# Performance work log

Hardware: AMD Instinct MI355X
Metric: run time of the kernel (lower is better)

## Reference

```python
import jax, jax.numpy as jnp
import numpy as np

N_NODES = 50000
N_EDGES = 800000
IN_DIM = 256
OUT_DIM = 64


def setup_inputs() -> dict:
    key = jax.random.key(0)
    k1, k2, k3, k4, k5 = jax.random.split(key, 5)
    h = jax.random.normal(k1, (N_NODES, IN_DIM), dtype=jnp.float32)
    # fc: Linear(in_dim, out_dim, bias=False) -> weight shape [out_dim, in_dim]
    W_fc = jax.random.normal(k2, (OUT_DIM, IN_DIM), dtype=jnp.float32) / np.sqrt(IN_DIM)
    # attn_fc: Linear(2*out_dim, 1, bias=False) -> weight shape [1, 2*out_dim]
    W_attn = jax.random.normal(k3, (1, 2 * OUT_DIM), dtype=jnp.float32) / np.sqrt(2 * OUT_DIM)
    src = jax.random.randint(k4, (N_EDGES,), 0, N_NODES, dtype=jnp.int64 if jax.config.read('jax_enable_x64') else jnp.int32).astype(jnp.int32)
    dst = jax.random.randint(k5, (N_EDGES,), 0, N_NODES, dtype=jnp.int32)
    return {"h": h, "W_fc": W_fc, "W_attn": W_attn, "src": src, "dst": dst}


def reference(h, W_fc, W_attn, src, dst):
    # z = self.fc(h)
    z = h @ W_fc.T                              # [N, D]
    # edge_attention: e = leaky_relu(attn_fc(cat(z_src, z_dst)))
    z_src = z[src]                              # [E, D] gather
    z_dst = z[dst]                              # [E, D] gather
    z2 = jnp.concatenate([z_src, z_dst], axis=1)  # [E, 2D]
    e = jax.nn.leaky_relu(z2 @ W_attn.T)[:, 0]  # [E], torch default slope 0.01
    # reduce_func: segment softmax over incoming edges per dst node
    n = h.shape[0]
    m = jax.ops.segment_max(e, dst, num_segments=n)        # [N] per-node max
    e_exp = jnp.exp(e - m[dst])                             # [E] stable exp
    denom = jax.ops.segment_sum(e_exp, dst, num_segments=n)  # [N]
    alpha = e_exp / jnp.maximum(denom, 1e-16)[dst]          # [E]
    # h' = sum_j alpha_ij * z_j
    out = jax.ops.segment_sum(alpha[:, None] * z_src, dst, num_segments=n)  # [N, D]
    return out
```

## Files before the change

kernel.cpp:

```cpp
#include <hip/hip_runtime.h>

#define N_NODES 50000
#define N_EDGES 800000
#define IN_DIM  256
#define OUT_DIM 64
#define BINW    128
#define NBINS   512
#define NBINS_USED ((N_NODES + BINW - 1) / BINW)
#define PB      112
#define CH4     ((N_EDGES / 4 + PB - 1) / PB)
#define NB_GEMM ((N_NODES + 63) / 64)
#define GRID_FUSED 896
#define CSRCAP  4096

typedef _Float16 f16;
typedef __attribute__((ext_vector_type(2))) __fp16 hf16x2;
typedef __attribute__((ext_vector_type(4))) _Float16 f16x4;
typedef __attribute__((ext_vector_type(8))) _Float16 f16x8;
typedef __attribute__((ext_vector_type(4))) float f32x4;

__device__ __forceinline__ unsigned int pack_sw(int s, float w) {
    f16 hw = (f16)w;
    unsigned short us;
    __builtin_memcpy(&us, &hw, 2);
    return ((unsigned int)s << 16) | us;
}
__device__ __forceinline__ float unpack_w(unsigned int e) {
    unsigned short us = (unsigned short)(e & 0xffffu);
    f16 hw;
    __builtin_memcpy(&hw, &us, 2);
    return (float)hw;
}


__global__ __launch_bounds__(256) void k_prep(const float* __restrict__ W,
                                              f16* __restrict__ Wh,
                                              int* __restrict__ binCount) {
    int idx = blockIdx.x * 256 + threadIdx.x;
    if (idx < (OUT_DIM * IN_DIM) / 4) {
        float4 v = ((const float4*)W)[idx];
        f16x4 p = { (f16)v.x, (f16)v.y, (f16)v.z, (f16)v.w };
        ((f16x4*)Wh)[idx] = p;
    }
    if (idx < NBINS) binCount[idx] = 0;
}

__global__ __launch_bounds__(256) void k_fused(const float* __restrict__ h,
                                               const f16* __restrict__ Wh,
                                               const float* __restrict__ Wa,
                                               const int* __restrict__ dst,
                                               f16* __restrict__ z,
                                               float* __restrict__ a_src,
                                               float* __restrict__ a_dst,
                                               int* __restrict__ binCount,
                                               int* __restrict__ base) {
    __shared__ int hist[NBINS];
    const int g = blockIdx.x;
    const int t = threadIdx.x;

    if ((g & 7) == 7) {
        const int pb = g >> 3;
        for (int b = t; b < NBINS; b += 256) hist[b] = 0;
        __syncthreads();
        const int s4 = pb * CH4;
        const int e4 = min(s4 + CH4, N_EDGES / 4);
        for (int i4 = s4 + t; i4 < e4; i4 += 256) {
            int4 dv = ((const int4*)dst)[i4];
            atomicAdd(&hist[dv.x >> 7], 1);
            atomicAdd(&hist[dv.y >> 7], 1);
            atomicAdd(&hist[dv.z >> 7], 1);
            atomicAdd(&hist[dv.w >> 7], 1);
        }
        __syncthreads();
        for (int b = t; b < NBINS; b += 256) {
            int c = hist[b];
            if (c) base[pb * NBINS + b] = atomicAdd(&binCount[b], c);
        }
        return;
    }

    const int gemm_id = g - (g >> 3);
    if (gemm_id >= NB_GEMM) return;

    const int row0  = gemm_id * 64;
    const int lane  = t & 63;
    const int wid   = t >> 6;
    const int cl    = lane & 15;
    const int khalf = lane >> 4;

    int arow = row0 + wid * 16 + cl;
    if (arow >= N_NODES) arow = N_NODES - 1;
    const float* hrow = h + (size_t)arow * IN_DIM;

    f32x4 acc[4] = {};

    #pragma unroll 4
    for (int kc = 0; kc < IN_DIM; kc += 32) {
        const int k0 = kc + khalf * 8;
        float4 va = *(const float4*)&hrow[k0];
        float4 vb = *(const float4*)&hrow[k0 + 4];
        union { hf16x2 h2[4]; f16x8 h8; } ua;
        ua.h2[0] = __builtin_amdgcn_cvt_pkrtz(va.x, va.y);
        ua.h2[1] = __builtin_amdgcn_cvt_pkrtz(va.z, va.w);
        ua.h2[2] = __builtin_amdgcn_cvt_pkrtz(vb.x, vb.y);
        ua.h2[3] = __builtin_amdgcn_cvt_pkrtz(vb.z, vb.w);
        f16x8 a = ua.h8;
        #pragma unroll
        for (int ct = 0; ct < 4; ++ct) {
            const int col = ct * 16 + cl;
            f16x8 b = *(const f16x8*)&Wh[col * 256 + k0];
            acc[ct] = __builtin_amdgcn_mfma_f32_16x16x32_f16(a, b, acc[ct], 0, 0, 0);
        }
    }

    const int rbase = row0 + wid * 16 + khalf * 4;
    #pragma unroll
    for (int ct = 0; ct < 4; ++ct) {
        #pragma unroll
        for (int r = 0; r < 4; ++r) {
            int row = rbase + r;
            if (row < N_NODES)
                z[(size_t)row * OUT_DIM + ct * 16 + cl] = (f16)acc[ct][r];
        }
    }

    float wa1[4], wa2[4];
    #pragma unroll
    for (int ct = 0; ct < 4; ++ct) {
        wa1[ct] = Wa[ct * 16 + cl];
        wa2[ct] = Wa[64 + ct * 16 + cl];
    }
    #pragma unroll
    for (int r = 0; r < 4; ++r) {
        float s1 = 0.f, s2 = 0.f;
        #pragma unroll
        for (int ct = 0; ct < 4; ++ct) {
            s1 += acc[ct][r] * wa1[ct];
            s2 += acc[ct][r] * wa2[ct];
        }
        #pragma unroll
        for (int off = 1; off < 16; off <<= 1) {
            s1 += __shfl_xor(s1, off);
            s2 += __shfl_xor(s2, off);
        }
        int row = rbase + r;
        if (cl == 0 && row < N_NODES) {
            a_src[row] = s1;
            a_dst[row] = s2;
        }
    }
}

__global__ __launch_bounds__(256) void k_place(const int* __restrict__ src,
                                               const int* __restrict__ dst,
                                               const int* __restrict__ binCount,
                                               const int* __restrict__ base,
                                               int* __restrict__ ebuf) {
    __shared__ int cursor[NBINS];
    const int pb = blockIdx.x;
    const int t  = threadIdx.x;

    if (t < 64) {
        int vals[8]; int run = 0;
        #pragma unroll
        for (int i = 0; i < 8; ++i) { int c = binCount[t * 8 + i]; vals[i] = run; run += c; }
        int incl = run;
        #pragma unroll
        for (int off = 1; off < 64; off <<= 1) {
            int u = __shfl_up(incl, off);
            if (t >= off) incl += u;
        }
        const int lex = incl - run;
        #pragma unroll
        for (int i = 0; i < 8; ++i) cursor[t * 8 + i] = lex + vals[i];
    }
    __syncthreads();
    for (int b = t; b < NBINS; b += 256) cursor[b] += base[pb * NBINS + b];
    __syncthreads();

    const int s4 = pb * CH4;
    const int e4 = min(s4 + CH4, N_EDGES / 4);
    for (int i4 = s4 + t; i4 < e4; i4 += 256) {
        int4 dv = ((const int4*)dst)[i4];
        int4 sv = ((const int4*)src)[i4];
        int slot;
        slot = atomicAdd(&cursor[dv.x >> 7], 1); ebuf[slot] = (sv.x << 7) | (dv.x & 127);
        slot = atomicAdd(&cursor[dv.y >> 7], 1); ebuf[slot] = (sv.y << 7) | (dv.y & 127);
        slot = atomicAdd(&cursor[dv.z >> 7], 1); ebuf[slot] = (sv.z << 7) | (dv.z & 127);
        slot = atomicAdd(&cursor[dv.w >> 7], 1); ebuf[slot] = (sv.w << 7) | (dv.w & 127);
    }
}

__global__ __launch_bounds__(1024) void k_binagg(const int* __restrict__ ebuf,
                                                 const int* __restrict__ binCount,
                                                 const float* __restrict__ a_src,
                                                 const float* __restrict__ a_dst,
                                                 const f16* __restrict__ z,
                                                 float* __restrict__ out) {
    __shared__ int cnt[BINW];
    __shared__ int rb[BINW];
    __shared__ int cur[BINW];
    __shared__ float adl[BINW];
    __shared__ unsigned int lcsr[CSRCAP];
    __shared__ int sh_estart;
    const int b    = blockIdx.x;
    const int t    = threadIdx.x;
    const int lane = t & 63;
    const int wid  = t >> 6;
    const int node0 = b * BINW;
    const int ecnt  = min(binCount[b], CSRCAP);

    if (t < 64) {
        int partial = 0;
        for (int i = t; i < b; i += 64) partial += binCount[i];
        #pragma unroll
        for (int off = 32; off; off >>= 1) partial += __shfl_xor(partial, off);
        if (t == 0) sh_estart = partial;
    }
    if (t < BINW) {
        cnt[t] = 0;
        int gd = node0 + t;
        adl[t] = (gd < N_NODES) ? a_dst[gd] : 0.f;
    }
    __syncthreads();
    const int estart = sh_estart;

    for (int i = t; i < ecnt; i += 1024)
        atomicAdd(&cnt[ebuf[estart + i] & (BINW - 1)], 1);
    __syncthreads();

    if (t < 64) {
        int v0 = cnt[t], v1 = cnt[t + 64];
        int i0 = v0;
        #pragma unroll
        for (int off = 1; off < 64; off <<= 1) {
            int u = __shfl_up(i0, off);
            if (t >= off) i0 += u;
        }
        int tot0 = __shfl(i0, 63);
        int i1 = v1;
        #pragma unroll
        for (int off = 1; off < 64; off <<= 1) {
            int u = __shfl_up(i1, off);
            if (t >= off) i1 += u;
        }
        int e0 = i0 - v0;
        int e1 = tot0 + i1 - v1;
        rb[t]       = e0;  cur[t]      = e0;
        rb[t + 64]  = e1;  cur[t + 64] = e1;
    }
    __syncthreads();

    for (int i = t; i < ecnt; i += 1024) {
        int pk = ebuf[estart + i];
        int ld = pk & (BINW - 1);
        int s  = pk >> 7;
        float u = a_src[s] + adl[ld];
        u = u > 0.f ? u : 0.01f * u;
        float w = __expf(u);
        int p = atomicAdd(&cur[ld], 1);
        lcsr[p] = pack_sw(s, w);
    }
    __syncthreads();

    const int grp = lane >> 3;
    const int cl  = lane & 7;
    #pragma unroll
    for (int i = 0; i < 8; ++i) {
        const int ld   = i * 16 + wid;
        const int node = node0 + ld;
        if (node >= N_NODES) continue;
        const int beg = rb[ld];
        const int deg = cnt[ld];

        float dn = 0.0f;
        float acc8[8] = {0.f, 0.f, 0.f, 0.f, 0.f, 0.f, 0.f, 0.f};

        for (int cb = 0; cb < deg; cb += 64) {
            const int rem = min(deg - cb, 64);
            if (lane < rem) dn += unpack_w(lcsr[beg + cb + lane]);
            const int kmax = (rem + 7) & ~7;
            for (int k = 0; k < kmax; k += 8) {
                const int ei = k + grp;
                unsigned int pe = (ei < rem) ? lcsr[beg + cb + ei] : 0u;
                int   sk = (int)(pe >> 16);
                float wk = unpack_w(pe);
                f16x8 zv = *(const f16x8*)&z[(size_t)sk * OUT_DIM + cl * 8];
                #pragma unroll
                for (int j = 0; j < 8; ++j)
                    acc8[j] = fmaf(wk, (float)zv[j], acc8[j]);
            }
        }

        #pragma unroll
        for (int off = 32; off; off >>= 1) dn += __shfl_xor(dn, off);
        #pragma unroll
        for (int off = 8; off < 64; off <<= 1) {
            #pragma unroll
            for (int j = 0; j < 8; ++j)
                acc8[j] += __shfl_xor(acc8[j], off);
        }

        if (lane < 8) {
            float inv = 1.0f / fmaxf(dn, 1e-16f);
            float4 o0 = make_float4(acc8[0] * inv, acc8[1] * inv, acc8[2] * inv, acc8[3] * inv);
            float4 o1 = make_float4(acc8[4] * inv, acc8[5] * inv, acc8[6] * inv, acc8[7] * inv);
            *(float4*)&out[(size_t)node * OUT_DIM + lane * 8]     = o0;
            *(float4*)&out[(size_t)node * OUT_DIM + lane * 8 + 4] = o1;
        }
    }
}


extern "C" void kernel_launch(void* const* d_in, const int* in_sizes, int n_in,
                              void* d_out, int out_size, void* d_ws, size_t ws_size,
                              hipStream_t stream) {
    const float* h      = (const float*)d_in[0];
    const float* W_fc   = (const float*)d_in[1];
    const float* W_attn = (const float*)d_in[2];
    const int*   src    = (const int*)d_in[3];
    const int*   dst    = (const int*)d_in[4];
    float* out = (float*)d_out;

    f16*   z        = (f16*)d_ws;
    f16*   Wh       = z + (size_t)N_NODES * OUT_DIM;
    float* a_src    = (float*)(Wh + OUT_DIM * IN_DIM);
    float* a_dst    = a_src + N_NODES;
    int*   binCount = (int*)(a_dst + N_NODES);
    int*   base     = binCount + NBINS;
    int*   ebuf     = base + PB * NBINS;

    k_prep<<<16, 256, 0, stream>>>(W_fc, Wh, binCount);
    k_fused<<<GRID_FUSED, 256, 0, stream>>>(h, Wh, W_attn, dst, z, a_src, a_dst, binCount, base);
    k_place<<<PB, 256, 0, stream>>>(src, dst, binCount, base, ebuf);
    k_binagg<<<NBINS_USED, 1024, 0, stream>>>(ebuf, binCount, a_src, a_dst, z, out);
}
```

Baseline: 79.94 us.

## Move histogram into prep kernel and fuse edge placement into GEMM kernel

The per-chunk dst histogram moves into the first kernel, which also converts W to fp16. The edge-placement pass then runs inside the fused GEMM kernel's spare blocks, with each block redundantly summing all chunk histograms to build its cursors. This removes one kernel launch and lets placement overlap the GEMM, and bin start/total arrays are written once for the aggregation kernel. The cost is that each placement block reads all PB×NBINS counts and scans them redundantly.

Measured after the change: 86.49 us. +8.2%, slower.

```diff
diff --git a/kernel.cpp b/kernel.cpp
--- a/kernel.cpp
+++ b/kernel.cpp
@@ -33,48 +33,112 @@
 }
 
 
-__global__ __launch_bounds__(256) void k_prep(const float* __restrict__ W,
-                                              f16* __restrict__ Wh,
-                                              int* __restrict__ binCount) {
-    int idx = blockIdx.x * 256 + threadIdx.x;
-    if (idx < (OUT_DIM * IN_DIM) / 4) {
-        float4 v = ((const float4*)W)[idx];
-        f16x4 p = { (f16)v.x, (f16)v.y, (f16)v.z, (f16)v.w };
-        ((f16x4*)Wh)[idx] = p;
-    }
-    if (idx < NBINS) binCount[idx] = 0;
+__global__ __launch_bounds__(1024) void k_prephist(const float* __restrict__ W,
+                                                   const int* __restrict__ dst,
+                                                   f16* __restrict__ Wh,
+                                                   int* __restrict__ base) {
+    const int g = blockIdx.x;
+    const int t = threadIdx.x;
+
+    if (g >= PB) {
+        int idx = (g - PB) * 1024 + t;
+        if (idx < (OUT_DIM * IN_DIM) / 4) {
+            float4 v = ((const float4*)W)[idx];
+            f16x4 p = { (f16)v.x, (f16)v.y, (f16)v.z, (f16)v.w };
+            ((f16x4*)Wh)[idx] = p;
+        }
+        return;
+    }
+
+    __shared__ int hist[NBINS];
+    if (t < NBINS) hist[t] = 0;
+    __syncthreads();
+    const int s4 = g * CH4;
+    const int e4 = min(s4 + CH4, N_EDGES / 4);
+    for (int i4 = s4 + t; i4 < e4; i4 += 1024) {
+        int4 dv = ((const int4*)dst)[i4];
+        atomicAdd(&hist[dv.x >> 7], 1);
+        atomicAdd(&hist[dv.y >> 7], 1);
+        atomicAdd(&hist[dv.z >> 7], 1);
+        atomicAdd(&hist[dv.w >> 7], 1);
+    }
+    __syncthreads();
+    if (t < NBINS) base[g * NBINS + t] = hist[t];
 }
 
 __global__ __launch_bounds__(256) void k_fused(const float* __restrict__ h,
                                                const f16* __restrict__ Wh,
                                                const float* __restrict__ Wa,
+                                               const int* __restrict__ src,
                                                const int* __restrict__ dst,
                                                f16* __restrict__ z,
                                                float* __restrict__ a_src,
                                                float* __restrict__ a_dst,
-                                               int* __restrict__ binCount,
-                                               int* __restrict__ base) {
-    __shared__ int hist[NBINS];
+                                               const int* __restrict__ base,
+                                               int* __restrict__ binStartG,
+                                               int* __restrict__ binTotalG,
+                                               int* __restrict__ ebuf) {
+    __shared__ int cursor[NBINS];
+    __shared__ int totalL[NBINS];
+    __shared__ int bstart[NBINS];
     const int g = blockIdx.x;
     const int t = threadIdx.x;
 
     if ((g & 7) == 7) {
         const int pb = g >> 3;
-        for (int b = t; b < NBINS; b += 256) hist[b] = 0;
+        int myPre0 = 0, myPre1 = 0;
+        {
+            int total = 0, pre = 0;
+            for (int q = 0; q < PB; ++q) {
+                int v = base[q * NBINS + t];
+                total += v;
+                if (q < pb) pre += v;
+            }
+            totalL[t] = total; myPre0 = pre;
+            total = 0; pre = 0;
+            for (int q = 0; q < PB; ++q) {
+                int v = base[q * NBINS + t + 256];
+                total += v;
+                if (q < pb) pre += v;
+            }
+            totalL[t + 256] = total; myPre1 = pre;
+        }
         __syncthreads();
+        if (t < 64) {
+            int vals[8]; int run = 0;
+            #pragma unroll
+            for (int i = 0; i < 8; ++i) { int c = totalL[t * 8 + i]; vals[i] = run; run += c; }
+            int incl = run;
+            #pragma unroll
+            for (int off = 1; off < 64; off <<= 1) {
+                int u = __shfl_up(incl, off);
+                if (t >= off) incl += u;
+            }
+            const int lex = incl - run;
+            #pragma unroll
+            for (int i = 0; i < 8; ++i) bstart[t * 8 + i] = lex + vals[i];
+        }
+        __syncthreads();
+        cursor[t]       = bstart[t] + myPre0;
+        cursor[t + 256] = bstart[t + 256] + myPre1;
+        if (g == 7) {
+            binStartG[t]       = bstart[t];
+            binStartG[t + 256] = bstart[t + 256];
+            binTotalG[t]       = totalL[t];
+            binTotalG[t + 256] = totalL[t + 256];
+        }
+        __syncthreads();
+
         const int s4 = pb * CH4;
         const int e4 = min(s4 + CH4, N_EDGES / 4);
         for (int i4 = s4 + t; i4 < e4; i4 += 256) {
             int4 dv = ((const int4*)dst)[i4];
-            atomicAdd(&hist[dv.x >> 7], 1);
-            atomicAdd(&hist[dv.y >> 7], 1);
-            atomicAdd(&hist[dv.z >> 7], 1);
-            atomicAdd(&hist[dv.w >> 7], 1);
-        }
-        __syncthreads();
-        for (int b = t; b < NBINS; b += 256) {
-            int c = hist[b];
-            if (c) base[pb * NBINS + b] = atomicAdd(&binCount[b], c);
+            int4 sv = ((const int4*)src)[i4];
+            int slot;
+            slot = atomicAdd(&cursor[dv.x >> 7], 1); ebuf[slot] = (sv.x << 7) | (dv.x & 127);
+            slot = atomicAdd(&cursor[dv.y >> 7], 1); ebuf[slot] = (sv.y << 7) | (dv.y & 127);
+            slot = atomicAdd(&cursor[dv.z >> 7], 1); ebuf[slot] = (sv.z << 7) | (dv.z & 127);
+            slot = atomicAdd(&cursor[dv.w >> 7], 1); ebuf[slot] = (sv.w << 7) | (dv.w & 127);
         }
         return;
     }
@@ -151,48 +215,9 @@
     }
 }
 
-__global__ __launch_bounds__(256) void k_place(const int* __restrict__ src,
-                                               const int* __restrict__ dst,
-                                               const int* __restrict__ binCount,
-                                               const int* __restrict__ base,
-                                               int* __restrict__ ebuf) {
-    __shared__ int cursor[NBINS];
-    const int pb = blockIdx.x;
-    const int t  = threadIdx.x;
-
-    if (t < 64) {
-        int vals[8]; int run = 0;
-        #pragma unroll
-        for (int i = 0; i < 8; ++i) { int c = binCount[t * 8 + i]; vals[i] = run; run += c; }
-        int incl = run;
-        #pragma unroll
-        for (int off = 1; off < 64; off <<= 1) {
-            int u = __shfl_up(incl, off);
-            if (t >= off) incl += u;
-        }
-        const int lex = incl - run;
-        #pragma unroll
-        for (int i = 0; i < 8; ++i) cursor[t * 8 + i] = lex + vals[i];
-    }
-    __syncthreads();
-    for (int b = t; b < NBINS; b += 256) cursor[b] += base[pb * NBINS + b];
-    __syncthreads();
-
-    const int s4 = pb * CH4;
-    const int e4 = min(s4 + CH4, N_EDGES / 4);
-    for (int i4 = s4 + t; i4 < e4; i4 += 256) {
-        int4 dv = ((const int4*)dst)[i4];
-        int4 sv = ((const int4*)src)[i4];
-        int slot;
-        slot = atomicAdd(&cursor[dv.x >> 7], 1); ebuf[slot] = (sv.x << 7) | (dv.x & 127);
-        slot = atomicAdd(&cursor[dv.y >> 7], 1); ebuf[slot] = (sv.y << 7) | (dv.y & 127);
-        slot = atomicAdd(&cursor[dv.z >> 7], 1); ebuf[slot] = (sv.z << 7) | (dv.z & 127);
-        slot = atomicAdd(&cursor[dv.w >> 7], 1); ebuf[slot] = (sv.w << 7) | (dv.w & 127);
-    }
-}
-
 __global__ __launch_bounds__(1024) void k_binagg(const int* __restrict__ ebuf,
-                                                 const int* __restrict__ binCount,
+                                                 const int* __restrict__ binStartG,
+                                                 const int* __restrict__ binTotalG,
                                                  const float* __restrict__ a_src,
                                                  const float* __restrict__ a_dst,
                                                  const f16* __restrict__ z,
@@ -202,28 +227,20 @@
     __shared__ int cur[BINW];
     __shared__ float adl[BINW];
     __shared__ unsigned int lcsr[CSRCAP];
-    __shared__ int sh_estart;
     const int b    = blockIdx.x;
     const int t    = threadIdx.x;
     const int lane = t & 63;
     const int wid  = t >> 6;
     const int node0 = b * BINW;
-    const int ecnt  = min(binCount[b], CSRCAP);
-
-    if (t < 64) {
-        int partial = 0;
-        for (int i = t; i < b; i += 64) partial += binCount[i];
-        #pragma unroll
-        for (int off = 32; off; off >>= 1) partial += __shfl_xor(partial, off);
-        if (t == 0) sh_estart = partial;
-    }
+    const int estart = binStartG[b];
+    const int ecnt   = min(binTotalG[b], CSRCAP);
+
     if (t < BINW) {
         cnt[t] = 0;
         int gd = node0 + t;
         adl[t] = (gd < N_NODES) ? a_dst[gd] : 0.f;
     }
     __syncthreads();
-    const int estart = sh_estart;
 
     for (int i = t; i < ecnt; i += 1024)
         atomicAdd(&cnt[ebuf[estart + i] & (BINW - 1)], 1);
@@ -326,12 +343,13 @@
     f16*   Wh       = z + (size_t)N_NODES * OUT_DIM;
     float* a_src    = (float*)(Wh + OUT_DIM * IN_DIM);
     float* a_dst    = a_src + N_NODES;
-    int*   binCount = (int*)(a_dst + N_NODES);
-    int*   base     = binCount + NBINS;
-    int*   ebuf     = base + PB * NBINS;
-
-    k_prep<<<16, 256, 0, stream>>>(W_fc, Wh, binCount);
-    k_fused<<<GRID_FUSED, 256, 0, stream>>>(h, Wh, W_attn, dst, z, a_src, a_dst, binCount, base);
-    k_place<<<PB, 256, 0, stream>>>(src, dst, binCount, base, ebuf);
-    k_binagg<<<NBINS_USED, 1024, 0, stream>>>(ebuf, binCount, a_src, a_dst, z, out);
-}
+    int*   base     = (int*)(a_dst + N_NODES);
+    int*   binStart = base + PB * NBINS;
+    int*   binTotal = binStart + NBINS;
+    int*   ebuf     = binTotal + NBINS;
+
+    k_prephist<<<PB + 4, 1024, 0, stream>>>(W_fc, dst, Wh, base);
+    k_fused<<<GRID_FUSED, 256, 0, stream>>>(h, Wh, W_attn, src, dst, z, a_src, a_dst,
+                                            base, binStart, binTotal, ebuf);
+    k_binagg<<<NBINS_USED, 1024, 0, stream>>>(ebuf, binStart, binTotal, a_src, a_dst, z, out);
+}
```
